# Optimization experiments

Hardware: AMD Instinct MI355X
Metric: run time of the kernel (lower is better)

Reference implementation:

```python
import jax, jax.numpy as jnp
import numpy as np

N = 100000
E_ADJ = 800000
E_RAY = 800000
IN_DIM = 2
HID = 64
HEADS = 2
NEG_SLOPE = 0.2  # PyG GATv2Conv default


def setup_inputs() -> dict:
    key = jax.random.key(0)
    ks = jax.random.split(key, 16)
    s = 0.1
    p = lambda k, shape: (jax.random.normal(k, shape, jnp.float32) * s)
    inp = {
        "x": jax.random.normal(ks[0], (N, IN_DIM), jnp.float32),
        "edge_adj": jax.random.randint(ks[1], (2, E_ADJ), 0, N, jnp.int32),
        "edge_ray": jax.random.randint(ks[2], (2, E_RAY), 0, N, jnp.int32),
        # layer 1 params, stacked over the 2 relation types [adjacent, ray]
        "l1_Wl": p(ks[3], (2, IN_DIM, HEADS * HID)),
        "l1_bl": jnp.zeros((2, HEADS * HID), jnp.float32),
        "l1_Wr": p(ks[4], (2, IN_DIM, HEADS * HID)),
        "l1_br": jnp.zeros((2, HEADS * HID), jnp.float32),
        "l1_att": p(ks[5], (2, HEADS, HID)),
        "l1_bias": jnp.zeros((2, HID), jnp.float32),
        # layer 2 params
        "l2_Wl": p(ks[6], (2, HID, HEADS * HID)),
        "l2_bl": jnp.zeros((2, HEADS * HID), jnp.float32),
        "l2_Wr": p(ks[7], (2, HID, HEADS * HID)),
        "l2_br": jnp.zeros((2, HEADS * HID), jnp.float32),
        "l2_att": p(ks[8], (2, HEADS, HID)),
        "l2_bias": jnp.zeros((2, HID), jnp.float32),
    }
    return inp


def _gatv2(x, src, dst, Wl, bl, Wr, br, att, bias):
    # GATv2Conv, concat=False, add_self_loops=False (PyG semantics)
    n = x.shape[0]
    H, C = att.shape
    xl = (x @ Wl + bl).reshape(n, H, C)  # source transform
    xr = (x @ Wr + br).reshape(n, H, C)  # target transform
    e = jax.nn.leaky_relu(xl[src] + xr[dst], NEG_SLOPE)  # [E,H,C]
    score = jnp.einsum('ehc,hc->eh', e, att)             # [E,H]
    # segment softmax over incoming edges per destination (per head)
    m = jax.ops.segment_max(score, dst, num_segments=n)  # only gathered at non-empty segs
    ex = jnp.exp(score - m[dst])
    denom = jax.ops.segment_sum(ex, dst, num_segments=n)
    alpha = ex / (denom[dst] + 1e-16)                    # [E,H]
    out = jax.ops.segment_sum(xl[src] * alpha[:, :, None], dst, num_segments=n)  # [N,H,C]
    return out.mean(axis=1) + bias                       # concat=False -> head mean


def _hetero_layer(x, ea, er, Wl, bl, Wr, br, att, bias):
    o_adj = _gatv2(x, ea[0], ea[1], Wl[0], bl[0], Wr[0], br[0], att[0], bias[0])
    o_ray = _gatv2(x, er[0], er[1], Wl[1], bl[1], Wr[1], br[1], att[1], bias[1])
    return 0.5 * (o_adj + o_ray)  # HeteroConv aggr='mean' over 2 relations


def reference(x, edge_adj, edge_ray,
              l1_Wl, l1_bl, l1_Wr, l1_br, l1_att, l1_bias,
              l2_Wl, l2_bl, l2_Wr, l2_br, l2_att, l2_bias):
    h = _hetero_layer(x, edge_adj, edge_ray, l1_Wl, l1_bl, l1_Wr, l1_br, l1_att, l1_bias)
    h = jax.nn.relu(h)
    out = _hetero_layer(h, edge_adj, edge_ray, l2_Wl, l2_bl, l2_Wr, l2_br, l2_att, l2_bias)
    return out
```

## Files before the change

### kernel.cpp

```cpp
#include <hip/hip_runtime.h>
#include <hip/hip_bf16.h>

typedef __hip_bfloat16 bf16;
typedef unsigned int uint;
typedef unsigned short ushort;
typedef __attribute__((ext_vector_type(8))) short short8;
typedef __attribute__((ext_vector_type(4))) float floatx4;

#define N_NODES 100000
#define N_PAD   100096
#define E_EDGES 800000
#define NBLK    98
#define EBLK    3125
#define RBLK    782

static __device__ __forceinline__ uint packbf(float a, float b) {
  bf16 x = __float2bfloat16(a), y = __float2bfloat16(b);
  ushort ux = *reinterpret_cast<ushort*>(&x);
  ushort uy = *reinterpret_cast<ushort*>(&y);
  return (uint)ux | ((uint)uy << 16);
}
static __device__ __forceinline__ float lo16(uint u) { return __uint_as_float(u << 16); }
static __device__ __forceinline__ float hi16(uint u) { return __uint_as_float(u & 0xffff0000u); }

static __device__ __forceinline__ float rsum16(float p) {
  p += __int_as_float(__builtin_amdgcn_update_dpp(
      0, __float_as_int(p), 0x128, 0xF, 0xF, false));
  p += __int_as_float(__builtin_amdgcn_update_dpp(
      0, __float_as_int(p), 0x124, 0xF, 0xF, false));
  p += __int_as_float(__builtin_amdgcn_update_dpp(
      0, __float_as_int(p), 0x122, 0xF, 0xF, false));
  p += __int_as_float(__builtin_amdgcn_update_dpp(
      0, __float_as_int(p), 0x121, 0xF, 0xF, false));
  return p;
}

__global__ __launch_bounds__(256) void rank_k(
    const int* __restrict__ dst0, const int* __restrict__ dst1,
    int* fi0, int* fi1, int* __restrict__ rk0, int* __restrict__ rk1) {
  int base = blockIdx.x * 256 + threadIdx.x;
  int rel = blockIdx.y;
  const int* dst = rel ? dst1 : dst0;
  int* fi = rel ? fi1 : fi0;
  int* rk = rel ? rk1 : rk0;
#pragma unroll
  for (int k = 0; k < 4; ++k) {
    int i = base + k * (RBLK * 256);
    if (i < E_EDGES) {
      int d = dst[i];
      rk[i] = atomicAdd(&fi[d], 1);
    }
  }
}

__global__ __launch_bounds__(256) void scat_rank_k(
    const int* __restrict__ src0, const int* __restrict__ dst0,
    const int* __restrict__ src1, const int* __restrict__ dst1,
    const int* __restrict__ rk0, const int* __restrict__ rk1,
    const int* __restrict__ rp0, const int* __restrict__ rp1,
    int2* __restrict__ csd0, int2* __restrict__ csd1) {
  int i = blockIdx.x * 256 + threadIdx.x;
  int rel = blockIdx.y;
  const int* src = rel ? src1 : src0;
  const int* dst = rel ? dst1 : dst0;
  const int* rk = rel ? rk1 : rk0;
  const int* rp = rel ? rp1 : rp0;
  int2* csd = rel ? csd1 : csd0;
  int d = dst[i];
  int s = src[i];
  int pos = rp[d] + rk[i];
  csd[pos] = make_int2(s, d);
}

__global__ void scan_blk_k(const int* __restrict__ deg0, const int* __restrict__ deg1,
                           int* rp0, int* rp1, int* bsum) {
  __shared__ int s[1024];
  int r = blockIdx.y;
  const int* deg = r ? deg1 : deg0;
  int* rp = r ? rp1 : rp0;
  int i = blockIdx.x * 1024 + threadIdx.x;
  int v = (i < N_NODES) ? deg[i] : 0;
  s[threadIdx.x] = v;
  __syncthreads();
  for (int off = 1; off < 1024; off <<= 1) {
    int t = (threadIdx.x >= off) ? s[threadIdx.x - off] : 0;
    __syncthreads();
    s[threadIdx.x] += t;
    __syncthreads();
  }
  if (i < N_NODES) rp[i] = s[threadIdx.x] - v;
  if (threadIdx.x == 1023) bsum[r * NBLK + blockIdx.x] = s[1023];
}

__global__ void scan_top_k(int* bsum, int* rp0, int* rp1) {
  __shared__ int s[128];
  int r = blockIdx.x;
  int v = (threadIdx.x < NBLK) ? bsum[r * NBLK + threadIdx.x] : 0;
  s[threadIdx.x] = v;
  __syncthreads();
  for (int off = 1; off < 128; off <<= 1) {
    int t = (threadIdx.x >= off) ? s[threadIdx.x - off] : 0;
    __syncthreads();
    s[threadIdx.x] += t;
    __syncthreads();
  }
  if (threadIdx.x < NBLK) bsum[r * NBLK + threadIdx.x] = s[threadIdx.x] - v;
  if (threadIdx.x == 127) (r ? rp1 : rp0)[N_NODES] = s[127];
}

__global__ void scan_add_k(const int* __restrict__ bsum,
                           int* rp0, int* rp1, int* fi0, int* fi1) {
  int r = blockIdx.y;
  int i = blockIdx.x * 1024 + threadIdx.x;
  if (i >= N_NODES) return;
  int* rp = r ? rp1 : rp0;
  int* fi = r ? fi1 : fi0;
  int val = rp[i] + bsum[r * NBLK + blockIdx.x];
  rp[i] = val;
  fi[i] = val;
}

__global__ void wprep_k(const float* __restrict__ Wl, const float* __restrict__ Wr,
                        short* __restrict__ WT,
                        const float* __restrict__ l1Wl, const float* __restrict__ l1bl,
                        const float* __restrict__ l1Wr, const float* __restrict__ l1br,
                        const float* __restrict__ l1att, float* __restrict__ L1C,
                        float* __restrict__ SCG) {
  if (blockIdx.x == 128) {
    int t = threadIdx.x;
    {
      int rel = t >> 7, c = t & 127;
      int ch = c >> 2, o = c & 3;
      float* g = SCG + rel * 768 + ch * 24;
      g[0 + o]  = l1bl[rel * 128 + c] + l1br[rel * 128 + c];
      g[4 + o]  = l1Wr[rel * 256 + c];
      g[8 + o]  = l1Wr[rel * 256 + 128 + c];
      g[12 + o] = l1Wl[rel * 256 + c];
      g[16 + o] = l1Wl[rel * 256 + 128 + c];
      g[20 + o] = l1att[rel * 128 + c];
    }
    if (t < 20) {
      int rel = t / 10, rem = t % 10, h = rem / 5, v = rem % 5;
      const float* a = l1att + rel * 128 + h * 64;
      float sum = 0.f;
      for (int c = 0; c < 64; ++c) {
        int cc = h * 64 + c;
        float val;
        if (v == 0)      val = l1bl[rel * 128 + cc] + l1br[rel * 128 + cc];
        else if (v == 1) val = l1Wr[rel * 256 + cc];
        else if (v == 2) val = l1Wr[rel * 256 + 128 + cc];
        else if (v == 3) val = l1Wl[rel * 256 + cc];
        else             val = l1Wl[rel * 256 + 128 + cc];
        sum += a[c] * val;
      }
      L1C[t] = sum;
    }
    return;
  }
  int id2 = blockIdx.x * 256 + threadIdx.x;
  int rel = id2 >> 14;
  int id = id2 & 16383;
  int c = id >> 6, k = id & 63;
  const float* W = (c < 128) ? (Wl + rel * 8192) : (Wr + rel * 8192);
  int cc = c & 127;
  bf16 b = __float2bfloat16(W[k * 128 + cc]);
  WT[rel * 16384 + c * 64 + k] = *reinterpret_cast<short*>(&b);
}

__global__ __launch_bounds__(256) void l1score_k(
    const int2* __restrict__ csd0, const int2* __restrict__ csd1,
    const float* __restrict__ x,
    const float* __restrict__ scg, const float* __restrict__ l1c,
    float4* __restrict__ EX4) {
  int rel = blockIdx.y;
  const int2* csd = rel ? csd1 : csd0;
  const float* sC = scg + rel * 768;
  const float* C = l1c + rel * 10;
  float q00 = C[0], qv00 = C[1], qv10 = C[2], qw00 = C[3], qw10 = C[4];
  float q01 = C[5], qv01 = C[6], qv11 = C[7], qw01 = C[8], qw11 = C[9];
  int i = blockIdx.x * 256 + threadIdx.x;
  int2 sd = csd[i];
  int s = sd.x, d = sd.y;
  float2 xs = *(const float2*)(x + 2 * s);
  float2 xd = *(const float2*)(x + 2 * d);
  float t0a = 0.f, t0b = 0.f, t1a = 0.f, t1b = 0.f;
#pragma unroll
  for (int ch = 0; ch < 32; ++ch) {
    const float4* cp = (const float4*)(sC + ch * 24);
    float4 bb = cp[0], v0 = cp[1], v1 = cp[2], w0 = cp[3], w1 = cp[4], aa = cp[5];
    float e0 = bb.x + xd.x * v0.x + xd.y * v1.x + xs.x * w0.x + xs.y * w1.x;
    float e1 = bb.y + xd.x * v0.y + xd.y * v1.y + xs.x * w0.y + xs.y * w1.y;
    float e2 = bb.z + xd.x * v0.z + xd.y * v1.z + xs.x * w0.z + xs.y * w1.z;
    float e3 = bb.w + xd.x * v0.w + xd.y * v1.w + xs.x * w0.w + xs.y * w1.w;
    if (ch < 16) {
      t0a = fmaf(aa.x, fabsf(e0), t0a); t0b = fmaf(aa.y, fabsf(e1), t0b);
      t0a = fmaf(aa.z, fabsf(e2), t0a); t0b = fmaf(aa.w, fabsf(e3), t0b);
    } else {
      t1a = fmaf(aa.x, fabsf(e0), t1a); t1b = fmaf(aa.y, fabsf(e1), t1b);
      t1a = fmaf(aa.z, fabsf(e2), t1a); t1b = fmaf(aa.w, fabsf(e3), t1b);
    }
  }
  float T0 = t0a + t0b, T1 = t1a + t1b;
  float lin0 = q00 + xd.x * qv00 + xd.y * qv10 + xs.x * qw00 + xs.y * qw10;
  float lin1 = q01 + xd.x * qv01 + xd.y * qv11 + xs.x * qw01 + xs.y * qw11;
  float p0 = fmaf(0.4f, T0, 0.6f * lin0);
  float p1 = fmaf(0.4f, T1, 0.6f * lin1);
  EX4[(size_t)rel * E_EDGES + i] = make_float4(__expf(p0), __expf(p1), xs.x, xs.y);
}

__global__ __launch_bounds__(256) void l1aggfin_k(
    const int* __restrict__ rp0, const int* __restrict__ rp1,
    const float4* __restrict__ EX4,
    const float* __restrict__ Wl, const float* __restrict__ bl,
    const float* __restrict__ bias, uint2* __restrict__ HB2) {
  __shared__ __align__(16) float sNA[64][12];
  int t = threadIdx.x;
  int g = blockIdx.x * 64 + (t >> 2);
  int k = t & 3;
  float p0 = 0.f, p1 = 0.f, p2 = 0.f, p3 = 0.f, p4 = 0.f, p5 = 0.f;
  float p6 = 0.f, p7 = 0.f, p8 = 0.f, p9 = 0.f, p10 = 0.f, p11 = 0.f;
  if (g < N_NODES) {
    {
      int beg = rp0[g], end = rp0[g + 1];
      for (int j = beg + k; j < end; j += 4) {
        float4 e = EX4[j];
        p0 += e.x; p1 = fmaf(e.x, e.z, p1); p2 = fmaf(e.x, e.w, p2);
        p3 += e.y; p4 = fmaf(e.y, e.z, p4); p5 = fmaf(e.y, e.w, p5);
      }
    }
    {
      const float4* E1 = EX4 + E_EDGES;
      int beg = rp1[g], end = rp1[g + 1];
      for (int j = beg + k; j < end; j += 4) {
        float4 e = E1[j];
        p6 += e.x; p7 = fmaf(e.x, e.z, p7); p8 = fmaf(e.x, e.w, p8);
        p9 += e.y; p10 = fmaf(e.y, e.z, p10); p11 = fmaf(e.y, e.w, p11);
      }
    }
  }
#define RED4(v) v += __shfl_xor(v, 1); v += __shfl_xor(v, 2);
  RED4(p0) RED4(p1) RED4(p2) RED4(p3) RED4(p4) RED4(p5)
  RED4(p6) RED4(p7) RED4(p8) RED4(p9) RED4(p10) RED4(p11)
#undef RED4
  {
    int dl = t >> 2;
    if (k == 0)      *(float4*)(&sNA[dl][0]) = make_float4(p0, p1, p2, p3);
    else if (k == 1) *(float4*)(&sNA[dl][4]) = make_float4(p4, p5, p6, p7);
    else if (k == 2) *(float4*)(&sNA[dl][8]) = make_float4(p8, p9, p10, p11);
  }
  __syncthreads();
#pragma unroll
  for (int rep = 0; rep < 4; ++rep) {
    int idx = rep * 256 + t;
    int dl = idx >> 4, l = idx & 15;
    int d = blockIdx.x * 64 + dl;
    if (d >= N_NODES) continue;
    int c0 = 4 * l;
    const float* na = sNA[dl];
    float out0 = 0.f, out1 = 0.f, out2 = 0.f, out3 = 0.f;
#pragma unroll
    for (int r = 0; r < 2; ++r) {
      float a0c = 0.f, a1c = 0.f, a2c = 0.f, a3c = 0.f;
#pragma unroll
      for (int h = 0; h < 2; ++h) {
        float den = na[r * 6 + h * 3 + 0];
        float A0  = na[r * 6 + h * 3 + 1];
        float A1  = na[r * 6 + h * 3 + 2];
        float inv = 1.f / (den + 1e-16f);
        float a0 = A0 * inv, a1 = A1 * inv, S = den * inv;
        float4 W0 = *(const float4*)(Wl + r * 256 + h * 64 + c0);
        float4 W1 = *(const float4*)(Wl + r * 256 + 128 + h * 64 + c0);
        float4 B  = *(const float4*)(bl + r * 128 + h * 64 + c0);
        a0c += a0 * W0.x + a1 * W1.x + S * B.x;
        a1c += a0 * W0.y + a1 * W1.y + S * B.y;
        a2c += a0 * W0.z + a1 * W1.z + S * B.z;
        a3c += a0 * W0.w + a1 * W1.w + S * B.w;
      }
      float4 bi = *(const float4*)(bias + r * 64 + c0);
      out0 += 0.5f * a0c + bi.x;
      out1 += 0.5f * a1c + bi.y;
      out2 += 0.5f * a2c + bi.z;
      out3 += 0.5f * a3c + bi.w;
    }
    out0 = fmaxf(0.5f * out0, 0.f); out1 = fmaxf(0.5f * out1, 0.f);
    out2 = fmaxf(0.5f * out2, 0.f); out3 = fmaxf(0.5f * out3, 0.f);
    HB2[(size_t)d * 16 + l] = make_uint2(packbf(out0, out1), packbf(out2, out3));
  }
}

__global__ __launch_bounds__(256) void mfma_t_k(const bf16* __restrict__ HB,
                                                const short* __restrict__ WTb,
                                                const float* __restrict__ blb,
                                                const float* __restrict__ brb,
                                                bf16* __restrict__ XL0,
                                                bf16* __restrict__ XR0,
                                                bf16* __restrict__ XL1,
                                                bf16* __restrict__ XR1) {
  __shared__ short sW[256 * 72];
  int rel = blockIdx.z;
  const short* WT = WTb + rel * 16384;
  const float* bl = blb + rel * 128;
  const float* br = brb + rel * 128;
  bf16* XLp = rel ? XL1 : XL0;
  bf16* XRp = rel ? XR1 : XR0;
  int t = threadIdx.x;
#pragma unroll
  for (int i = 0; i < 8; ++i) {
    int chunk = t + i * 256;
    int c = chunk >> 3, off = (chunk & 7) * 8;
    *(short8*)(&sW[c * 72 + off]) = *(const short8*)(WT + chunk * 8);
  }
  __syncthreads();
  int wave = t >> 6, lane = t & 63;
  int q = lane >> 4, m = lane & 15;
  int rowbase = blockIdx.x * 128 + wave * 32;
  short8 afr[2][2];
#pragma unroll
  for (int rt = 0; rt < 2; ++rt)
#pragma unroll
    for (int kh = 0; kh < 2; ++kh) {
      size_t row = (size_t)(rowbase + rt * 16 + m);
      afr[rt][kh] = *(const short8*)((const short*)HB + row * 64 + kh * 32 + q * 8);
    }
  for (int ct = 0; ct < 16; ++ct) {
    int col = ct * 16 + m;
    short8 b0 = *(const short8*)(&sW[col * 72 + q * 8]);
    short8 b1 = *(const short8*)(&sW[col * 72 + 32 + q * 8]);
    int c0 = ct * 16 + q * 4;
    int c128 = c0 & 127;
    const float* bp = (ct < 8) ? bl : br;
    bf16* X = (ct < 8) ? XLp : XRp;
    float4 bv = *(const float4*)(bp + c128);
#pragma unroll
    for (int rt = 0; rt < 2; ++rt) {
      floatx4 acc = {0.f, 0.f, 0.f, 0.f};
      acc = __builtin_amdgcn_mfma_f32_16x16x32_bf16(b0, afr[rt][0], acc, 0, 0, 0);
      acc = __builtin_amdgcn_mfma_f32_16x16x32_bf16(b1, afr[rt][1], acc, 0, 0, 0);
      int node = rowbase + rt * 16 + m;
      if (node < N_NODES) {
        uint u0 = packbf(acc[0] + bv.x, acc[1] + bv.y);
        uint u1 = packbf(acc[2] + bv.z, acc[3] + bv.w);
        *(uint2*)((ushort*)X + (size_t)node * 128 + c128) = make_uint2(u0, u1);
      }
    }
  }
}

struct EdgeAcc { float a0, a1, a2, a3, den; };

static __device__ __forceinline__ void edge_step(
    uint2 u, float xr0, float xr1, float xr2, float xr3,
    float at0, float at1, float at2, float at3, float q06, EdgeAcc& A) {
  float x0 = lo16(u.x), x1 = hi16(u.x), x2 = lo16(u.y), x3 = hi16(u.y);
  float e0 = x0 + xr0, e1 = x1 + xr1, e2 = x2 + xr2, e3 = x3 + xr3;
  float sa = at0 * fabsf(e0);
  sa = fmaf(at1, fabsf(e1), sa);
  sa = fmaf(at2, fabsf(e2), sa);
  sa = fmaf(at3, fabsf(e3), sa);
  float sx = at0 * x0;
  sx = fmaf(at1, x1, sx);
  sx = fmaf(at2, x2, sx);
  sx = fmaf(at3, x3, sx);
  float p = fmaf(0.6f, sx, 0.4f * sa);
  p = rsum16(p);
  float ex = __expf(p + q06);
  A.den += ex;
  A.a0 = fmaf(ex, x0, A.a0);
  A.a1 = fmaf(ex, x1, A.a1);
  A.a2 = fmaf(ex, x2, A.a2);
  A.a3 = fmaf(ex, x3, A.a3);
}

__global__ __launch_bounds__(256) void aggf_k(
    const int* __restrict__ rp0, const int2* __restrict__ csd0,
    const int* __restrict__ rp1, const int2* __restrict__ csd1,
    const bf16* __restrict__ XL0, const bf16* __restrict__ XR0,
    const bf16* __restrict__ XL1, const bf16* __restrict__ XR1,
    const float* __restrict__ att,
    const float* __restrict__ bias,
    float* __restrict__ outf) {
  int d = (blockIdx.x * 256 + threadIdx.x) >> 6;
  int lane = threadIdx.x & 63;
  if (d >= N_NODES) return;
  int half = lane >> 5;
  int l = lane & 31;
  int beg0 = rp0[d], end0 = rp0[d + 1];
  int beg1 = rp1[d], end1 = rp1[d + 1];
  const float* at = att + 4 * l;
  const float* bt = att + 128 + 4 * l;
  float at0 = at[0], at1 = at[1], at2 = at[2], at3 = at[3];
  float bt0 = bt[0], bt1 = bt[1], bt2 = bt[2], bt3 = bt[3];
  uint2 ur0 = *(const uint2*)(XR0 + (size_t)d * 128 + 4 * l);
  uint2 ur1 = *(const uint2*)(XR1 + (size_t)d * 128 + 4 * l);
  float xa0 = lo16(ur0.x), xa1 = hi16(ur0.x), xa2 = lo16(ur0.y), xa3 = hi16(ur0.y);
  float xb0 = lo16(ur1.x), xb1 = hi16(ur1.x), xb2 = lo16(ur1.y), xb3 = hi16(ur1.y);
  float qa = at0 * xa0; qa = fmaf(at1, xa1, qa);
  qa = fmaf(at2, xa2, qa); qa = fmaf(at3, xa3, qa);
  qa = 0.6f * rsum16(qa);
  float qb = bt0 * xb0; qb = fmaf(bt1, xb1, qb);
  qb = fmaf(bt2, xb2, qb); qb = fmaf(bt3, xb3, qb);
  qb = 0.6f * rsum16(qb);
  EdgeAcc A = {0.f, 0.f, 0.f, 0.f, 0.f};
  EdgeAcc B = {0.f, 0.f, 0.f, 0.f, 0.f};
  {
    int j = beg0 + half;
    for (; j + 6 < end0; j += 8) {
      int s0 = csd0[j].x, s1 = csd0[j + 2].x;
      int s2 = csd0[j + 4].x, s3 = csd0[j + 6].x;
      uint2 u0 = *(const uint2*)(XL0 + (size_t)s0 * 128 + 4 * l);
      uint2 u1 = *(const uint2*)(XL0 + (size_t)s1 * 128 + 4 * l);
      uint2 u2 = *(const uint2*)(XL0 + (size_t)s2 * 128 + 4 * l);
      uint2 u3 = *(const uint2*)(XL0 + (size_t)s3 * 128 + 4 * l);
      edge_step(u0, xa0, xa1, xa2, xa3, at0, at1, at2, at3, qa, A);
      edge_step(u1, xa0, xa1, xa2, xa3, at0, at1, at2, at3, qa, A);
      edge_step(u2, xa0, xa1, xa2, xa3, at0, at1, at2, at3, qa, A);
      edge_step(u3, xa0, xa1, xa2, xa3, at0, at1, at2, at3, qa, A);
    }
    for (; j < end0; j += 2) {
      int s = csd0[j].x;
      uint2 u = *(const uint2*)(XL0 + (size_t)s * 128 + 4 * l);
      edge_step(u, xa0, xa1, xa2, xa3, at0, at1, at2, at3, qa, A);
    }
  }
  {
    int j = beg1 + half;
    for (; j + 6 < end1; j += 8) {
      int s0 = csd1[j].x, s1 = csd1[j + 2].x;
      int s2 = csd1[j + 4].x, s3 = csd1[j + 6].x;
      uint2 u0 = *(const uint2*)(XL1 + (size_t)s0 * 128 + 4 * l);
      uint2 u1 = *(const uint2*)(XL1 + (size_t)s1 * 128 + 4 * l);
      uint2 u2 = *(const uint2*)(XL1 + (size_t)s2 * 128 + 4 * l);
      uint2 u3 = *(const uint2*)(XL1 + (size_t)s3 * 128 + 4 * l);
      edge_step(u0, xb0, xb1, xb2, xb3, bt0, bt1, bt2, bt3, qb, B);
      edge_step(u1, xb0, xb1, xb2, xb3, bt0, bt1, bt2, bt3, qb, B);
      edge_step(u2, xb0, xb1, xb2, xb3, bt0, bt1, bt2, bt3, qb, B);
      edge_step(u3, xb0, xb1, xb2, xb3, bt0, bt1, bt2, bt3, qb, B);
    }
    for (; j < end1; j += 2) {
      int s = csd1[j].x;
      uint2 u = *(const uint2*)(XL1 + (size_t)s * 128 + 4 * l);
      edge_step(u, xb0, xb1, xb2, xb3, bt0, bt1, bt2, bt3, qb, B);
    }
  }
#define C32(v) v += __shfl_xor(v, 32);
  C32(A.den) C32(A.a0) C32(A.a1) C32(A.a2) C32(A.a3)
  C32(B.den) C32(B.a0) C32(B.a1) C32(B.a2) C32(B.a3)
#undef C32
  float invA = 1.f / (A.den + 1e-16f);
  float invB = 1.f / (B.den + 1e-16f);
  A.a0 *= invA; A.a1 *= invA; A.a2 *= invA; A.a3 *= invA;
  B.a0 *= invB; B.a1 *= invB; B.a2 *= invB; B.a3 *= invB;
  float t0 = 0.5f * (A.a0 + __shfl_xor(A.a0, 16));
  float t1 = 0.5f * (A.a1 + __shfl_xor(A.a1, 16));
  float t2 = 0.5f * (A.a2 + __shfl_xor(A.a2, 16));
  float t3 = 0.5f * (A.a3 + __shfl_xor(A.a3, 16));
  float u0 = 0.5f * (B.a0 + __shfl_xor(B.a0, 16));
  float u1 = 0.5f * (B.a1 + __shfl_xor(B.a1, 16));
  float u2 = 0.5f * (B.a2 + __shfl_xor(B.a2, 16));
  float u3 = 0.5f * (B.a3 + __shfl_xor(B.a3, 16));
  if (lane >= 16) return;
  int c0 = 4 * lane;
  t0 += bias[c0]; t1 += bias[c0 + 1]; t2 += bias[c0 + 2]; t3 += bias[c0 + 3];
  u0 += bias[64 + c0]; u1 += bias[64 + c0 + 1];
  u2 += bias[64 + c0 + 2]; u3 += bias[64 + c0 + 3];
  float v0 = 0.5f * (t0 + u0);
  float v1 = 0.5f * (t1 + u1);
  float v2 = 0.5f * (t2 + u2);
  float v3 = 0.5f * (t3 + u3);
  *(float4*)(outf + (size_t)d * 64 + c0) = make_float4(v0, v1, v2, v3);
}

extern "C" void kernel_launch(void* const* d_in, const int* in_sizes, int n_in,
                              void* d_out, int out_size, void* d_ws, size_t ws_size,
                              hipStream_t stream) {
  const float* x       = (const float*)d_in[0];
  const int*   e_adj   = (const int*)d_in[1];
  const int*   e_ray   = (const int*)d_in[2];
  const float* l1_Wl   = (const float*)d_in[3];
  const float* l1_bl   = (const float*)d_in[4];
  const float* l1_Wr   = (const float*)d_in[5];
  const float* l1_br   = (const float*)d_in[6];
  const float* l1_att  = (const float*)d_in[7];
  const float* l1_bias = (const float*)d_in[8];
  const float* l2_Wl   = (const float*)d_in[9];
  const float* l2_bl   = (const float*)d_in[10];
  const float* l2_Wr   = (const float*)d_in[11];
  const float* l2_br   = (const float*)d_in[12];
  const float* l2_att  = (const float*)d_in[13];
  const float* l2_bias = (const float*)d_in[14];
  float* out = (float*)d_out;

  char* w = (char*)d_ws;
  size_t off = 0;
  auto alloc = [&](size_t bytes) -> char* {
    char* p = w + off;
    off += (bytes + 255) & ~(size_t)255;
    return p;
  };
  bf16* XL0  = (bf16*)alloc((size_t)N_PAD * 128 * 2);
  bf16* XR0  = (bf16*)alloc((size_t)N_PAD * 128 * 2);
  bf16* XL1  = (bf16*)alloc((size_t)N_PAD * 128 * 2);
  bf16* XR1  = (bf16*)alloc((size_t)N_PAD * 128 * 2);
  bf16* HB   = (bf16*)alloc((size_t)N_PAD * 64 * 2);
  short* WT  = (short*)alloc(2 * 16384 * 2);
  int* RP0   = (int*)alloc((size_t)(N_NODES + 1) * 4);
  int* RP1   = (int*)alloc((size_t)(N_NODES + 1) * 4);
  int* FI0   = (int*)alloc((size_t)N_NODES * 4);
  int* FI1   = (int*)alloc((size_t)N_NODES * 4);
  int2* CSD0 = (int2*)alloc((size_t)E_EDGES * 8);
  int2* CSD1 = (int2*)alloc((size_t)E_EDGES * 8);
  int* BSUM  = (int*)alloc(2 * NBLK * 4);
  float* L1C = (float*)alloc(20 * 4);
  float* SCG = (float*)alloc(2 * 768 * 4);

  float4* EX4 = (float4*)XL0;
  int* RK0    = (int*)XL1;
  int* RK1    = (int*)((char*)XL1 + 3200000);

  const int* src_adj = e_adj;
  const int* dst_adj = e_adj + E_EDGES;
  const int* src_ray = e_ray;
  const int* dst_ray = e_ray + E_EDGES;

  const int WNB = (N_NODES * 64) / 256;
  const int MB  = N_PAD / 128;

  size_t fispan = (size_t)((char*)FI1 - (char*)FI0) + (size_t)N_NODES * 4;
  hipMemsetAsync(FI0, 0, fispan, stream);
  rank_k<<<dim3(RBLK, 2), 256, 0, stream>>>(dst_adj, dst_ray, FI0, FI1, RK0, RK1);
  scan_blk_k<<<dim3(NBLK, 2), 1024, 0, stream>>>(FI0, FI1, RP0, RP1, BSUM);
  scan_top_k<<<2, 128, 0, stream>>>(BSUM, RP0, RP1);
  scan_add_k<<<dim3(NBLK, 2), 1024, 0, stream>>>(BSUM, RP0, RP1, FI0, FI1);
  scat_rank_k<<<dim3(EBLK, 2), 256, 0, stream>>>(src_adj, dst_adj, src_ray, dst_ray,
                                                 RK0, RK1, RP0, RP1, CSD0, CSD1);
  wprep_k<<<129, 256, 0, stream>>>(l2_Wl, l2_Wr, WT,
                                   l1_Wl, l1_bl, l1_Wr, l1_br, l1_att, L1C, SCG);

  l1score_k<<<dim3(EBLK, 2), 256, 0, stream>>>(CSD0, CSD1, x, SCG, L1C, EX4);
  l1aggfin_k<<<(N_NODES + 63) / 64, 256, 0, stream>>>(RP0, RP1, EX4,
                                                      l1_Wl, l1_bl, l1_bias,
                                                      (uint2*)HB);

  mfma_t_k<<<dim3(MB, 1, 2), 256, 0, stream>>>(HB, WT, l2_bl, l2_br,
                                               XL0, XR0, XL1, XR1);
  aggf_k<<<WNB, 256, 0, stream>>>(RP0, CSD0, RP1, CSD1, XL0, XR0, XL1, XR1,
                                  l2_att, l2_bias, out);
}
```

Baseline: 409.9 us.

## Build CSR with histogram then atomic scatter, wave-shuffle scan, parallel L1 constants

The CSR build now runs a plain atomic histogram first and then scatters each edge by atomically claiming a slot from the scanned offsets. This drops the per-edge rank array and its write and read traffic. The block scan now uses wave shuffles instead of a shared-memory Hillis-Steele loop with many barriers, and the layer-1 attention constants are computed by 160 threads with a shared-memory reduction instead of 20 serial threads. The catch is that edge order within each CSR row becomes nondeterministic, so floating-point summation order may vary from run to run.

```diff
diff --git a/kernel.cpp b/kernel.cpp
--- a/kernel.cpp
+++ b/kernel.cpp
@@ -35,61 +35,68 @@
   return p;
 }
 
-__global__ __launch_bounds__(256) void rank_k(
+__global__ __launch_bounds__(256) void hist_k(
     const int* __restrict__ dst0, const int* __restrict__ dst1,
-    int* fi0, int* fi1, int* __restrict__ rk0, int* __restrict__ rk1) {
-  int base = blockIdx.x * 256 + threadIdx.x;
+    int* fi0, int* fi1) {
+  int i = blockIdx.x * 256 + threadIdx.x;
   int rel = blockIdx.y;
   const int* dst = rel ? dst1 : dst0;
   int* fi = rel ? fi1 : fi0;
-  int* rk = rel ? rk1 : rk0;
+  atomicAdd(&fi[dst[i]], 1);
+}
+
+__global__ __launch_bounds__(256) void scat_atomic_k(
+    const int* __restrict__ src0, const int* __restrict__ dst0,
+    const int* __restrict__ src1, const int* __restrict__ dst1,
+    int* fi0, int* fi1, int2* __restrict__ csd0, int2* __restrict__ csd1) {
+  int base = blockIdx.x * 256 + threadIdx.x;
+  int rel = blockIdx.y;
+  const int* src = rel ? src1 : src0;
+  const int* dst = rel ? dst1 : dst0;
+  int* fi = rel ? fi1 : fi0;
+  int2* csd = rel ? csd1 : csd0;
 #pragma unroll
   for (int k = 0; k < 4; ++k) {
     int i = base + k * (RBLK * 256);
     if (i < E_EDGES) {
-      int d = dst[i];
-      rk[i] = atomicAdd(&fi[d], 1);
-    }
-  }
-}
-
-__global__ __launch_bounds__(256) void scat_rank_k(
-    const int* __restrict__ src0, const int* __restrict__ dst0,
-    const int* __restrict__ src1, const int* __restrict__ dst1,
-    const int* __restrict__ rk0, const int* __restrict__ rk1,
-    const int* __restrict__ rp0, const int* __restrict__ rp1,
-    int2* __restrict__ csd0, int2* __restrict__ csd1) {
-  int i = blockIdx.x * 256 + threadIdx.x;
-  int rel = blockIdx.y;
-  const int* src = rel ? src1 : src0;
-  const int* dst = rel ? dst1 : dst0;
-  const int* rk = rel ? rk1 : rk0;
-  const int* rp = rel ? rp1 : rp0;
-  int2* csd = rel ? csd1 : csd0;
-  int d = dst[i];
-  int s = src[i];
-  int pos = rp[d] + rk[i];
-  csd[pos] = make_int2(s, d);
+      int d = dst[i], s = src[i];
+      int p = atomicAdd(&fi[d], 1);
+      csd[p] = make_int2(s, d);
+    }
+  }
 }
 
 __global__ void scan_blk_k(const int* __restrict__ deg0, const int* __restrict__ deg1,
                            int* rp0, int* rp1, int* bsum) {
-  __shared__ int s[1024];
+  __shared__ int ws[16];
   int r = blockIdx.y;
   const int* deg = r ? deg1 : deg0;
   int* rp = r ? rp1 : rp0;
   int i = blockIdx.x * 1024 + threadIdx.x;
   int v = (i < N_NODES) ? deg[i] : 0;
-  s[threadIdx.x] = v;
+  int lane = threadIdx.x & 63, wid = threadIdx.x >> 6;
+  int s = v;
+#pragma unroll
+  for (int off = 1; off < 64; off <<= 1) {
+    int t = __shfl_up(s, off);
+    if (lane >= off) s += t;
+  }
+  if (lane == 63) ws[wid] = s;
   __syncthreads();
-  for (int off = 1; off < 1024; off <<= 1) {
-    int t = (threadIdx.x >= off) ? s[threadIdx.x - off] : 0;
-    __syncthreads();
-    s[threadIdx.x] += t;
-    __syncthreads();
-  }
-  if (i < N_NODES) rp[i] = s[threadIdx.x] - v;
-  if (threadIdx.x == 1023) bsum[r * NBLK + blockIdx.x] = s[1023];
+  if (wid == 0) {
+    int wv = (lane < 16) ? ws[lane] : 0;
+#pragma unroll
+    for (int off = 1; off < 16; off <<= 1) {
+      int t = __shfl_up(wv, off);
+      if (lane >= off) wv += t;
+    }
+    if (lane < 16) ws[lane] = wv;
+  }
+  __syncthreads();
+  int base = wid ? ws[wid - 1] : 0;
+  int incl = base + s;
+  if (i < N_NODES) rp[i] = incl - v;
+  if (threadIdx.x == 1023) bsum[r * NBLK + blockIdx.x] = incl;
 }
 
 __global__ void scan_top_k(int* bsum, int* rp0, int* rp1) {
@@ -127,6 +134,7 @@
                         const float* __restrict__ l1att, float* __restrict__ L1C,
                         float* __restrict__ SCG) {
   if (blockIdx.x == 128) {
+    __shared__ float lps[20][8];
     int t = threadIdx.x;
     {
       int rel = t >> 7, c = t & 127;
@@ -139,21 +147,29 @@
       g[16 + o] = l1Wl[rel * 256 + 128 + c];
       g[20 + o] = l1att[rel * 128 + c];
     }
-    if (t < 20) {
-      int rel = t / 10, rem = t % 10, h = rem / 5, v = rem % 5;
+    if (t < 160) {
+      int v5 = t >> 3, kk = t & 7;
+      int rel = v5 / 10, rem = v5 % 10, h = rem / 5, vv = rem % 5;
       const float* a = l1att + rel * 128 + h * 64;
       float sum = 0.f;
-      for (int c = 0; c < 64; ++c) {
+      for (int c = kk * 8; c < kk * 8 + 8; ++c) {
         int cc = h * 64 + c;
         float val;
-        if (v == 0)      val = l1bl[rel * 128 + cc] + l1br[rel * 128 + cc];
-        else if (v == 1) val = l1Wr[rel * 256 + cc];
-        else if (v == 2) val = l1Wr[rel * 256 + 128 + cc];
-        else if (v == 3) val = l1Wl[rel * 256 + cc];
-        else             val = l1Wl[rel * 256 + 128 + cc];
+        if (vv == 0)      val = l1bl[rel * 128 + cc] + l1br[rel * 128 + cc];
+        else if (vv == 1) val = l1Wr[rel * 256 + cc];
+        else if (vv == 2) val = l1Wr[rel * 256 + 128 + cc];
+        else if (vv == 3) val = l1Wl[rel * 256 + cc];
+        else              val = l1Wl[rel * 256 + 128 + cc];
         sum += a[c] * val;
       }
-      L1C[t] = sum;
+      lps[v5][kk] = sum;
+    }
+    __syncthreads();
+    if (t < 20) {
+      float s = 0.f;
+#pragma unroll
+      for (int j = 0; j < 8; ++j) s += lps[t][j];
+      L1C[t] = s;
     }
     return;
   }
@@ -514,8 +530,6 @@
   float* SCG = (float*)alloc(2 * 768 * 4);
 
   float4* EX4 = (float4*)XL0;
-  int* RK0    = (int*)XL1;
-  int* RK1    = (int*)((char*)XL1 + 3200000);
 
   const int* src_adj = e_adj;
   const int* dst_adj = e_adj + E_EDGES;
@@ -527,12 +541,12 @@
 
   size_t fispan = (size_t)((char*)FI1 - (char*)FI0) + (size_t)N_NODES * 4;
   hipMemsetAsync(FI0, 0, fispan, stream);
-  rank_k<<<dim3(RBLK, 2), 256, 0, stream>>>(dst_adj, dst_ray, FI0, FI1, RK0, RK1);
+  hist_k<<<dim3(EBLK, 2), 256, 0, stream>>>(dst_adj, dst_ray, FI0, FI1);
   scan_blk_k<<<dim3(NBLK, 2), 1024, 0, stream>>>(FI0, FI1, RP0, RP1, BSUM);
   scan_top_k<<<2, 128, 0, stream>>>(BSUM, RP0, RP1);
   scan_add_k<<<dim3(NBLK, 2), 1024, 0, stream>>>(BSUM, RP0, RP1, FI0, FI1);
-  scat_rank_k<<<dim3(EBLK, 2), 256, 0, stream>>>(src_adj, dst_adj, src_ray, dst_ray,
-                                                 RK0, RK1, RP0, RP1, CSD0, CSD1);
+  scat_atomic_k<<<dim3(RBLK, 2), 256, 0, stream>>>(src_adj, dst_adj, src_ray,
+                                                   dst_ray, FI0, FI1, CSD0, CSD1);
   wprep_k<<<129, 256, 0, stream>>>(l2_Wl, l2_Wr, WT,
                                    l1_Wl, l1_bl, l1_Wr, l1_br, l1_att, L1C, SCG);
 
```

Result: slower. 501.0 us (+22.2%).
